# Optimization experiments

Measured on AMD Instinct MI355X. Metric: run time of the kernel, lower is better.

Reference implementation:

```python
import jax, jax.numpy as jnp
import numpy as np
import math

D_MODEL = 512
NHEAD = 8
D_K = D_MODEL // NHEAD
WINDOW = 128
BATCH = 1
SEQ = 4096
NEG = -1e9  # matches torch masked_fill value


def setup_inputs() -> dict:
    key = jax.random.key(0)
    ks = jax.random.split(key, 9)
    s = 1.0 / math.sqrt(D_MODEL)
    return {
        "x": jax.random.normal(ks[0], (BATCH, SEQ, D_MODEL), dtype=jnp.float32),
        "wq": jax.random.uniform(ks[1], (D_MODEL, D_MODEL), jnp.float32, -s, s),
        "bq": jax.random.uniform(ks[2], (D_MODEL,), jnp.float32, -s, s),
        "wk": jax.random.uniform(ks[3], (D_MODEL, D_MODEL), jnp.float32, -s, s),
        "bk": jax.random.uniform(ks[4], (D_MODEL,), jnp.float32, -s, s),
        "wv": jax.random.uniform(ks[5], (D_MODEL, D_MODEL), jnp.float32, -s, s),
        "bv": jax.random.uniform(ks[6], (D_MODEL,), jnp.float32, -s, s),
        "wo": jax.random.uniform(ks[7], (D_MODEL, D_MODEL), jnp.float32, -s, s),
        "bo": jax.random.uniform(ks[8], (D_MODEL,), jnp.float32, -s, s),
    }


def reference(x, wq, bq, wk, bk, wv, bv, wo, bo):
    B, S, D = x.shape
    # projections -> (B, H, S, d_k)
    q = (x @ wq.T + bq).reshape(B, S, NHEAD, D_K).transpose(0, 2, 1, 3)
    k = (x @ wk.T + bk).reshape(B, S, NHEAD, D_K).transpose(0, 2, 1, 3)
    v = (x @ wv.T + bv).reshape(B, S, NHEAD, D_K).transpose(0, 2, 1, 3)
    # dense scores, band-masked (faithful to original: full S x S)
    scores = jnp.einsum('bhqd,bhkd->bhqk', q, k) / math.sqrt(D_K)
    idx = jnp.arange(S)
    band = jnp.abs(idx[:, None] - idx[None, :]) <= WINDOW  # (S, S)
    scores = jnp.where(band[None, None], scores, NEG)
    attn = jax.nn.softmax(scores, axis=-1)  # (B, H, S, S)
    ctx = jnp.einsum('bhqk,bhkd->bhqd', attn, v)
    ctx = ctx.transpose(0, 2, 1, 3).reshape(B, S, D)
    out = ctx @ wo.T + bo
    return out, attn
```

## Files before the change

kernel.cpp:

```cpp
#include <hip/hip_runtime.h>
#include <hip/hip_bf16.h>
#include <math.h>

#define S 4096
#define D 512
#define H 8
#define DK 64
#define WIN 128

typedef __attribute__((ext_vector_type(8))) short bf16x8;
typedef __attribute__((ext_vector_type(4))) float f32x4;

__device__ __forceinline__ unsigned short f2bf(float f) {
    __hip_bfloat16 h = __float2bfloat16(f);
    return *(unsigned short*)&h;
}
__device__ __forceinline__ float bf2f(unsigned short u) {
    unsigned int x = ((unsigned int)u) << 16;
    return __uint_as_float(x);
}

__global__ __launch_bounds__(256) void conv_bf16_kernel(
    const float* __restrict__ x,
    const float* __restrict__ wq, const float* __restrict__ wk,
    const float* __restrict__ wv, const float* __restrict__ wo,
    unsigned short* __restrict__ xb,
    unsigned short* __restrict__ wqb, unsigned short* __restrict__ wkb,
    unsigned short* __restrict__ wvb, unsigned short* __restrict__ wob)
{
    const float* src; unsigned short* dst; int n;
    switch (blockIdx.y) {
        case 0:  src = x;  dst = xb;  n = S * D; break;
        case 1:  src = wq; dst = wqb; n = D * D; break;
        case 2:  src = wk; dst = wkb; n = D * D; break;
        case 3:  src = wv; dst = wvb; n = D * D; break;
        default: src = wo; dst = wob; n = D * D; break;
    }
    const int i = (blockIdx.x * 256 + threadIdx.x) * 8;
    if (i >= n) return;
    float4 a = *(const float4*)&src[i];
    float4 b = *(const float4*)&src[i + 4];
    ushort4 o0 = {f2bf(a.x), f2bf(a.y), f2bf(a.z), f2bf(a.w)};
    ushort4 o1 = {f2bf(b.x), f2bf(b.y), f2bf(b.z), f2bf(b.w)};
    *(ushort4*)&dst[i]     = o0;
    *(ushort4*)&dst[i + 4] = o1;
}

__device__ __forceinline__ void mfma_gemm_body(
    const unsigned short* __restrict__ A,
    const unsigned short* __restrict__ W16,
    const float* __restrict__ bias,
    float* __restrict__ C,
    unsigned short* __restrict__ CB,
    unsigned short* __restrict__ CBT)
{
    __shared__ unsigned short Bs[64][264];

    const int tid  = threadIdx.x;
    const int m0   = blockIdx.x * 128;
    const int n0   = blockIdx.y * 64;
    const int wv   = tid >> 6;
    const int lane = tid & 63;
    const int l16  = lane & 15;
    const int klo  = (lane >> 4) * 8;

    const unsigned short* arow0 = &A[(size_t)(m0 + wv * 32 + l16) * 512 + klo];
    const unsigned short* arow1 = arow0 + 16 * 512;

    f32x4 acc[2][4];
    #pragma unroll
    for (int r = 0; r < 2; ++r)
        #pragma unroll
        for (int nf = 0; nf < 4; ++nf)
            acc[r][nf] = (f32x4){0.f, 0.f, 0.f, 0.f};

    #pragma unroll
    for (int half = 0; half < 2; ++half) {
        const int kbase = half * 256;
        #pragma unroll
        for (int it = 0; it < 8; ++it) {
            const int c   = tid + it * 256;
            const int row = c >> 5;
            const int kc  = (c & 31) * 8;
            *(bf16x8*)&Bs[row][kc] =
                *(const bf16x8*)&W16[(size_t)(n0 + row) * 512 + kbase + kc];
        }
        __syncthreads();

        #pragma unroll 4
        for (int kb = 0; kb < 256; kb += 32) {
            bf16x8 a0 = *(const bf16x8*)&arow0[kbase + kb];
            bf16x8 a1 = *(const bf16x8*)&arow1[kbase + kb];
            #pragma unroll
            for (int nf = 0; nf < 4; ++nf) {
                bf16x8 b = *(const bf16x8*)&Bs[nf * 16 + l16][kb + klo];
                acc[0][nf] = __builtin_amdgcn_mfma_f32_16x16x32_bf16(a0, b, acc[0][nf], 0, 0, 0);
                acc[1][nf] = __builtin_amdgcn_mfma_f32_16x16x32_bf16(a1, b, acc[1][nf], 0, 0, 0);
            }
        }
        __syncthreads();
    }

    const int r0 = (lane >> 4) * 4;
    #pragma unroll
    for (int r = 0; r < 2; ++r) {
        #pragma unroll
        for (int nf = 0; nf < 4; ++nf) {
            const int col = n0 + nf * 16 + l16;
            const float bb = bias[col];
            if (CBT) {
                ushort4 o;
                o.x = f2bf(acc[r][nf][0] + bb);
                o.y = f2bf(acc[r][nf][1] + bb);
                o.z = f2bf(acc[r][nf][2] + bb);
                o.w = f2bf(acc[r][nf][3] + bb);
                const int row0 = m0 + wv * 32 + r * 16 + r0;
                *(ushort4*)&CBT[(size_t)col * 4096 + row0] = o;
            } else {
                #pragma unroll
                for (int vv = 0; vv < 4; ++vv) {
                    const int row = m0 + wv * 32 + r * 16 + r0 + vv;
                    const float val = acc[r][nf][vv] + bb;
                    if (C)  C [(size_t)row * 512 + col] = val;
                    if (CB) CB[(size_t)row * 512 + col] = f2bf(val);
                }
            }
        }
    }
}

__global__ __launch_bounds__(256) void proj3_kernel(
    const unsigned short* __restrict__ xb,
    const unsigned short* __restrict__ wqb, const float* __restrict__ bq,
    const unsigned short* __restrict__ wkb, const float* __restrict__ bk,
    const unsigned short* __restrict__ wvb, const float* __restrict__ bv,
    unsigned short* __restrict__ qb, unsigned short* __restrict__ kb,
    unsigned short* __restrict__ vT)
{
    if (blockIdx.z == 0)
        mfma_gemm_body(xb, wqb, bq, nullptr, qb, nullptr);
    else if (blockIdx.z == 1)
        mfma_gemm_body(xb, wkb, bk, nullptr, kb, nullptr);
    else
        mfma_gemm_body(xb, wvb, bv, nullptr, nullptr, vT);
}

__global__ __launch_bounds__(256) void outproj_kernel(
    const unsigned short* __restrict__ ctxb,
    const unsigned short* __restrict__ wob, const float* __restrict__ bo,
    float* __restrict__ out)
{
    mfma_gemm_body(ctxb, wob, bo, out, nullptr, nullptr);
}

__global__ __launch_bounds__(256) void band_attn_kernel(
    const unsigned short* __restrict__ qb, const unsigned short* __restrict__ kb,
    const unsigned short* __restrict__ vT,
    float* __restrict__ attn, unsigned short* __restrict__ ctxb)
{
    __shared__ __align__(16) unsigned short KV[64][72];
    __shared__ __align__(16) unsigned short Pb[16][344];
    __shared__ float rinvs[16];

    const int tid = threadIdx.x;
    const int h  = blockIdx.y;
    const int q0 = blockIdx.x * 16;
    const int w0 = q0 - 128;

    const int wv   = tid >> 6;
    const int lane = tid & 63;
    const int l16  = lane & 15;
    const int klo  = (lane >> 4) * 8;
    const int r0   = (lane >> 4) * 4;

    const unsigned short* qrow = &qb[(size_t)(q0 + l16) * 512 + h * 64 + klo];
    const bf16x8 aq0 = *(const bf16x8*)&qrow[0];
    const bf16x8 aq1 = *(const bf16x8*)&qrow[32];

    const int lr = tid >> 2;
    const int ld = (tid & 3) * 16;

    for (int ch = 0; ch < 5; ++ch) {
        const int c0 = w0 + ch * 64;
        if (c0 + 64 <= 0 || c0 >= S) continue;
        __syncthreads();
        {
            const int krow = min(max(c0 + lr, 0), S - 1);
            const unsigned short* src = &kb[(size_t)krow * 512 + h * 64 + ld];
            *(bf16x8*)&KV[lr][ld]     = *(const bf16x8*)&src[0];
            *(bf16x8*)&KV[lr][ld + 8] = *(const bf16x8*)&src[8];
        }
        __syncthreads();

        f32x4 acc = (f32x4){0.f, 0.f, 0.f, 0.f};
        bf16x8 b0 = *(const bf16x8*)&KV[wv * 16 + l16][klo];
        bf16x8 b1 = *(const bf16x8*)&KV[wv * 16 + l16][32 + klo];
        acc = __builtin_amdgcn_mfma_f32_16x16x32_bf16(aq0, b0, acc, 0, 0, 0);
        acc = __builtin_amdgcn_mfma_f32_16x16x32_bf16(aq1, b1, acc, 0, 0, 0);
        #pragma unroll
        for (int vv = 0; vv < 4; ++vv)
            Pb[r0 + vv][ch * 64 + wv * 16 + l16] = f2bf(acc[vv] * 0.125f);
    }
    __syncthreads();

    {
        const int r   = tid >> 4;
        const int lx  = tid & 15;
        const int i   = q0 + r;
        const int lo = max(i - WIN, 0) - w0;
        const int hi = min(i + WIN, S - 1) - w0;

        float m = -1e30f;
        for (int c = lo + lx; c <= hi; c += 16) m = fmaxf(m, bf2f(Pb[r][c]));
        m = fmaxf(m, __shfl_xor(m, 1));
        m = fmaxf(m, __shfl_xor(m, 2));
        m = fmaxf(m, __shfl_xor(m, 4));
        m = fmaxf(m, __shfl_xor(m, 8));

        float sum = 0.f;
        for (int c = lx; c < 320; c += 16) {
            unsigned short pe = 0;
            if (c >= lo && c <= hi) {
                float e = __expf(bf2f(Pb[r][c]) - m);
                sum += e;
                pe = f2bf(e);
            }
            Pb[r][c] = pe;
        }
        sum += __shfl_xor(sum, 1);
        sum += __shfl_xor(sum, 2);
        sum += __shfl_xor(sum, 4);
        sum += __shfl_xor(sum, 8);
        if (lx == 0) rinvs[r] = 1.0f / sum;
    }

    f32x4 pacc = (f32x4){0.f, 0.f, 0.f, 0.f};
    const int dd = tid >> 2;
    const int sc = (tid & 3) * 16;
    const unsigned short* vtd = &vT[((size_t)h * 64 + dd) * 4096];
    for (int ch = 0; ch < 5; ++ch) {
        const int c0 = w0 + ch * 64;
        if (c0 + 64 <= 0 || c0 >= S) continue;
        __syncthreads();
        {
            const int offs = min(max(c0 + sc, 0), S - 16);
            *(bf16x8*)&KV[dd][sc]     = *(const bf16x8*)&vtd[offs];
            *(bf16x8*)&KV[dd][sc + 8] = *(const bf16x8*)&vtd[offs + 8];
        }
        __syncthreads();

        #pragma unroll
        for (int kk = 0; kk < 64; kk += 32) {
            bf16x8 a = *(const bf16x8*)&Pb[l16][ch * 64 + kk + klo];
            bf16x8 b = *(const bf16x8*)&KV[wv * 16 + l16][kk + klo];
            pacc = __builtin_amdgcn_mfma_f32_16x16x32_bf16(a, b, pacc, 0, 0, 0);
        }
    }

    #pragma unroll
    for (int vv = 0; vv < 4; ++vv) {
        const int row = q0 + r0 + vv;
        ctxb[(size_t)row * 512 + h * 64 + wv * 16 + l16] =
            f2bf(pacc[vv] * rinvs[r0 + vv]);
    }

    float* rowbase = attn + (size_t)h * S * S;
    #pragma unroll 1
    for (int r = 0; r < 16; ++r) {
        const int i = q0 + r;
        float* rowp = rowbase + (size_t)i * S;
        const int lo = max(i - WIN, 0) - w0;
        const int hi = min(i + WIN, S - 1) - w0;
        const float rv = rinvs[r];
        #pragma unroll
        for (int t = 0; t < 4; ++t) {
            const int c4 = (tid + t * 256) << 2;
            const int lc = c4 - w0;
            float4 o;
            if (lc >= lo && lc + 3 <= hi) {
                ushort4 p = *(const ushort4*)&Pb[r][lc];
                o.x = bf2f(p.x) * rv; o.y = bf2f(p.y) * rv;
                o.z = bf2f(p.z) * rv; o.w = bf2f(p.w) * rv;
            } else if (lc + 3 < lo || lc > hi) {
                o = make_float4(0.f, 0.f, 0.f, 0.f);
            } else {
                o.x = (lc + 0 >= lo && lc + 0 <= hi) ? bf2f(Pb[r][lc + 0]) * rv : 0.f;
                o.y = (lc + 1 >= lo && lc + 1 <= hi) ? bf2f(Pb[r][lc + 1]) * rv : 0.f;
                o.z = (lc + 2 >= lo && lc + 2 <= hi) ? bf2f(Pb[r][lc + 2]) * rv : 0.f;
                o.w = (lc + 3 >= lo && lc + 3 <= hi) ? bf2f(Pb[r][lc + 3]) * rv : 0.f;
            }
            *(float4*)&rowp[c4] = o;
        }
    }
}

extern "C" void kernel_launch(void* const* d_in, const int* in_sizes, int n_in,
                              void* d_out, int out_size, void* d_ws, size_t ws_size,
                              hipStream_t stream)
{
    (void)in_sizes; (void)n_in; (void)out_size; (void)ws_size;
    const float* x  = (const float*)d_in[0];
    const float* wq = (const float*)d_in[1];
    const float* bq = (const float*)d_in[2];
    const float* wk = (const float*)d_in[3];
    const float* bk = (const float*)d_in[4];
    const float* wv = (const float*)d_in[5];
    const float* bv = (const float*)d_in[6];
    const float* wo = (const float*)d_in[7];
    const float* bo = (const float*)d_in[8];

    float* out  = (float*)d_out;
    float* attn = out + (size_t)S * D;

    unsigned short* xb   = (unsigned short*)d_ws;
    unsigned short* qb   = xb   + (size_t)S * D;
    unsigned short* kb   = qb   + (size_t)S * D;
    unsigned short* ctxb = kb   + (size_t)S * D;
    unsigned short* vT   = ctxb + (size_t)S * D;
    unsigned short* wqb  = vT   + (size_t)S * D;
    unsigned short* wkb  = wqb  + (size_t)D * D;
    unsigned short* wvb  = wkb  + (size_t)D * D;
    unsigned short* wob  = wvb  + (size_t)D * D;

    conv_bf16_kernel<<<dim3(1024, 5), 256, 0, stream>>>(
        x, wq, wk, wv, wo, xb, wqb, wkb, wvb, wob);
    proj3_kernel<<<dim3(32, 8, 3), 256, 0, stream>>>(
        xb, wqb, bq, wkb, bk, wvb, bv, qb, kb, vT);
    band_attn_kernel<<<dim3(256, 8), 256, 0, stream>>>(qb, kb, vT, attn, ctxb);
    outproj_kernel<<<dim3(32, 8), 256, 0, stream>>>(ctxb, wob, bo, out);
}
```

Measured before the change: 149.8 us.

## Use wave-private K/V tiles and interleave attn row stores with V loads

Each wave now loads only the 16 K rows and 16 V^T rows it consumes itself, so the block-wide barriers around the K and V chunk loads are removed. The V-chunk global loads are issued first, then a few rows of the dense attn output are written while those loads are in flight, and only then is the MFMA for that chunk run. This aims to cut barrier stalls and hide V load latency behind the large attn store stream. The cost is an uneven spread of store work across the chunk loop and more complex control flow.

```diff
diff --git a/kernel.cpp b/kernel.cpp
--- a/kernel.cpp
+++ b/kernel.cpp
@@ -173,25 +173,22 @@
     const int klo  = (lane >> 4) * 8;
     const int r0   = (lane >> 4) * 4;
 
+    const int l16s = lane & 15;
+    const int ds0  = (lane >> 4) * 16;
+
     const unsigned short* qrow = &qb[(size_t)(q0 + l16) * 512 + h * 64 + klo];
     const bf16x8 aq0 = *(const bf16x8*)&qrow[0];
     const bf16x8 aq1 = *(const bf16x8*)&qrow[32];
 
-    const int lr = tid >> 2;
-    const int ld = (tid & 3) * 16;
-
     for (int ch = 0; ch < 5; ++ch) {
         const int c0 = w0 + ch * 64;
         if (c0 + 64 <= 0 || c0 >= S) continue;
-        __syncthreads();
         {
-            const int krow = min(max(c0 + lr, 0), S - 1);
-            const unsigned short* src = &kb[(size_t)krow * 512 + h * 64 + ld];
-            *(bf16x8*)&KV[lr][ld]     = *(const bf16x8*)&src[0];
-            *(bf16x8*)&KV[lr][ld + 8] = *(const bf16x8*)&src[8];
-        }
-        __syncthreads();
-
+            const int krow = min(max(c0 + wv * 16 + l16s, 0), S - 1);
+            const unsigned short* src = &kb[(size_t)krow * 512 + h * 64 + ds0];
+            *(bf16x8*)&KV[wv * 16 + l16s][ds0]     = *(const bf16x8*)&src[0];
+            *(bf16x8*)&KV[wv * 16 + l16s][ds0 + 8] = *(const bf16x8*)&src[8];
+        }
         f32x4 acc = (f32x4){0.f, 0.f, 0.f, 0.f};
         bf16x8 b0 = *(const bf16x8*)&KV[wv * 16 + l16][klo];
         bf16x8 b1 = *(const bf16x8*)&KV[wv * 16 + l16][32 + klo];
@@ -233,40 +230,10 @@
         sum += __shfl_xor(sum, 8);
         if (lx == 0) rinvs[r] = 1.0f / sum;
     }
-
-    f32x4 pacc = (f32x4){0.f, 0.f, 0.f, 0.f};
-    const int dd = tid >> 2;
-    const int sc = (tid & 3) * 16;
-    const unsigned short* vtd = &vT[((size_t)h * 64 + dd) * 4096];
-    for (int ch = 0; ch < 5; ++ch) {
-        const int c0 = w0 + ch * 64;
-        if (c0 + 64 <= 0 || c0 >= S) continue;
-        __syncthreads();
-        {
-            const int offs = min(max(c0 + sc, 0), S - 16);
-            *(bf16x8*)&KV[dd][sc]     = *(const bf16x8*)&vtd[offs];
-            *(bf16x8*)&KV[dd][sc + 8] = *(const bf16x8*)&vtd[offs + 8];
-        }
-        __syncthreads();
-
-        #pragma unroll
-        for (int kk = 0; kk < 64; kk += 32) {
-            bf16x8 a = *(const bf16x8*)&Pb[l16][ch * 64 + kk + klo];
-            bf16x8 b = *(const bf16x8*)&KV[wv * 16 + l16][kk + klo];
-            pacc = __builtin_amdgcn_mfma_f32_16x16x32_bf16(a, b, pacc, 0, 0, 0);
-        }
-    }
-
-    #pragma unroll
-    for (int vv = 0; vv < 4; ++vv) {
-        const int row = q0 + r0 + vv;
-        ctxb[(size_t)row * 512 + h * 64 + wv * 16 + l16] =
-            f2bf(pacc[vv] * rinvs[r0 + vv]);
-    }
+    __syncthreads();
 
     float* rowbase = attn + (size_t)h * S * S;
-    #pragma unroll 1
-    for (int r = 0; r < 16; ++r) {
+    auto write_row = [&](int r) {
         const int i = q0 + r;
         float* rowp = rowbase + (size_t)i * S;
         const int lo = max(i - WIN, 0) - w0;
@@ -291,6 +258,41 @@
             }
             *(float4*)&rowp[c4] = o;
         }
+    };
+
+    f32x4 pacc = (f32x4){0.f, 0.f, 0.f, 0.f};
+    const unsigned short* vtd = &vT[((size_t)h * 64 + wv * 16 + l16s) * 4096];
+    int wrow = 0;
+    for (int ch = 0; ch < 5; ++ch) {
+        const int c0 = w0 + ch * 64;
+        const bool live = (c0 + 64 > 0) && (c0 < S);
+        bf16x8 v0, v1;
+        if (live) {
+            const int offs = min(max(c0 + ds0, 0), S - 16);
+            v0 = *(const bf16x8*)&vtd[offs];
+            v1 = *(const bf16x8*)&vtd[offs + 8];
+        }
+        #pragma unroll 1
+        for (int k2 = 0; k2 < 3 && wrow < 16; ++k2, ++wrow) write_row(wrow);
+        if (live) {
+            *(bf16x8*)&KV[wv * 16 + l16s][ds0]     = v0;
+            *(bf16x8*)&KV[wv * 16 + l16s][ds0 + 8] = v1;
+            #pragma unroll
+            for (int kk = 0; kk < 64; kk += 32) {
+                bf16x8 a = *(const bf16x8*)&Pb[l16][ch * 64 + kk + klo];
+                bf16x8 b = *(const bf16x8*)&KV[wv * 16 + l16][kk + klo];
+                pacc = __builtin_amdgcn_mfma_f32_16x16x32_bf16(a, b, pacc, 0, 0, 0);
+            }
+        }
+    }
+    #pragma unroll 1
+    while (wrow < 16) write_row(wrow++);
+
+    #pragma unroll
+    for (int vv = 0; vv < 4; ++vv) {
+        const int row = q0 + r0 + vv;
+        ctxb[(size_t)row * 512 + h * 64 + wv * 16 + l16] =
+            f2bf(pacc[vv] * rinvs[r0 + vv]);
     }
 }
 
```

After: 148.9 us. No clear change (-0.6%).
